# Kernel optimization log

Hardware: AMD Instinct MI355X
Metric: run time of the kernel (lower is better)

The kernel has to match this reference:

```python
import jax, jax.numpy as jnp
import numpy as np

N_USER = 100000
N_ITEM = 200000
N_NODES = N_USER + N_ITEM
NNZ = 4000000
EMB = 64
N_LAYERS = 3
BATCH = 4096


def setup_inputs() -> dict:
    key = jax.random.key(0)
    ks = jax.random.split(key, 12)
    inp = {
        'users': jax.random.randint(ks[0], (BATCH,), 0, N_USER, dtype=jnp.int32),
        'pos_items': jax.random.randint(ks[1], (BATCH,), 0, N_ITEM, dtype=jnp.int32),
        'neg_items': jax.random.randint(ks[2], (BATCH,), 0, N_ITEM, dtype=jnp.int32),
        'row': jax.random.randint(ks[3], (NNZ,), 0, N_NODES, dtype=jnp.int32),
        'col': jax.random.randint(ks[4], (NNZ,), 0, N_NODES, dtype=jnp.int32),
        'vals': jax.random.uniform(ks[5], (NNZ,), dtype=jnp.float32),
        'user_emb': 0.1 * jax.random.normal(ks[6], (N_USER, EMB), dtype=jnp.float32),
        'item_emb': 0.1 * jax.random.normal(ks[7], (N_ITEM, EMB), dtype=jnp.float32),
        'W_gc': 0.1 * jax.random.normal(ks[8], (N_LAYERS, EMB, EMB), dtype=jnp.float32),
        'b_gc': 0.1 * jax.random.normal(ks[9], (N_LAYERS, EMB), dtype=jnp.float32),
        'W_bi': 0.1 * jax.random.normal(ks[10], (N_LAYERS, EMB, EMB), dtype=jnp.float32),
        'b_bi': 0.1 * jax.random.normal(ks[11], (N_LAYERS, EMB), dtype=jnp.float32),
    }
    return inp


def _l2_normalize(x, eps=1e-12):
    # matches torch F.normalize(p=2, dim=1): x / max(||x||, eps)
    n = jnp.sqrt(jnp.sum(x * x, axis=1, keepdims=True))
    return x / jnp.maximum(n, eps)


def reference(users, pos_items, neg_items, row, col, vals, user_emb, item_emb, W_gc, b_gc, W_bi, b_bi):
    B = users.shape[0]
    # sparse adjacency propagation: side = A_hat @ [user_emb; item_emb]
    emb = jnp.concatenate([user_emb, item_emb], axis=0)          # [N, d]
    msgs = vals[:, None] * emb[col]                               # [nnz, d]
    side = jax.ops.segment_sum(msgs, row, num_segments=N_NODES)  # [N, d]

    u_side = side[users]                                          # [B, d]
    i_side = jnp.concatenate([side[N_USER + pos_items], side[N_USER + neg_items]], axis=0)
    small_side = jnp.concatenate([u_side, i_side], axis=0)        # [3B, d]
    ego = jnp.concatenate([user_emb[users], item_emb[pos_items], item_emb[neg_items]], axis=0)

    all_embeddings = [ego]
    for k in range(N_LAYERS):
        sum_e = small_side @ W_gc[k] + b_gc[k]
        bi = (ego * small_side) @ W_bi[k] + b_bi[k]
        ego = jax.nn.leaky_relu(sum_e + bi, negative_slope=0.2)
        all_embeddings.append(_l2_normalize(ego))

    all_e = jnp.concatenate(all_embeddings, axis=1)               # [3B, d*(L+1)]
    u_g = all_e[:B]
    i_g = all_e[B:]
    pos_g = i_g[:B]
    neg_g = i_g[B:]
    return (u_g, pos_g, neg_g)
```

## Files before the change

kernel.cpp:

```cpp
#include <hip/hip_runtime.h>

#define N_USER   100000
#define N_ITEM   200000
#define N_NODES  300000
#define NNZ      4000000
#define EMB      64
#define N_LAYERS 3
#define BATCH    4096
#define NSLOT    (3*BATCH)
#define MAXE     96
#define HCAP     768


__global__ void k_setup(const int* __restrict__ users,
                        const int* __restrict__ pos,
                        const int* __restrict__ neg,
                        int* __restrict__ slot_of_node,
                        int* __restrict__ count) {
    int i = blockIdx.x * blockDim.x + threadIdx.x;
    if (i >= NSLOT) return;
    count[i] = 0;
    int node;
    if (i < BATCH)            node = users[i];
    else if (i < 2 * BATCH)   node = N_USER + pos[i - BATCH];
    else                      node = N_USER + neg[i - 2 * BATCH];
    slot_of_node[node] = i;
}

__global__ void __launch_bounds__(256) k_build(
        const int* __restrict__ row,
        const int* __restrict__ col,
        const float* __restrict__ vals,
        const int* __restrict__ slot_of_node,
        int* __restrict__ count,
        int* __restrict__ csr_col,
        float* __restrict__ csr_val) {
    __shared__ int ls_e[HCAP];
    __shared__ int ls_s[HCAP];
    __shared__ int cnt;
    int tid = threadIdx.x;
    if (tid == 0) cnt = 0;
    __syncthreads();

    const int4* rows4 = (const int4*)row;
    const int nt4 = NNZ / 4;
    int base4 = blockIdx.x * 1024;

    int4 r[4]; bool ok[4];
    #pragma unroll
    for (int q = 0; q < 4; ++q) {
        int t = base4 + q * 256 + tid;
        ok[q] = t < nt4;
        r[q] = rows4[ok[q] ? t : 0];
    }
    int s[16];
    #pragma unroll
    for (int q = 0; q < 4; ++q) {
        s[q * 4 + 0] = slot_of_node[r[q].x];
        s[q * 4 + 1] = slot_of_node[r[q].y];
        s[q * 4 + 2] = slot_of_node[r[q].z];
        s[q * 4 + 3] = slot_of_node[r[q].w];
    }
    #pragma unroll
    for (int q = 0; q < 4; ++q) {
        if (!ok[q]) continue;
        int e = (base4 + q * 256 + tid) * 4;
        #pragma unroll
        for (int i = 0; i < 4; ++i) {
            int si = s[q * 4 + i];
            if (si >= 0) {
                int p = atomicAdd(&cnt, 1);
                if (p < HCAP) { ls_e[p] = e + i; ls_s[p] = si; }
                else {
                    int pp = atomicAdd(&count[si], 1);
                    if (pp < MAXE) {
                        csr_col[(size_t)si * MAXE + pp] = col[e + i];
                        csr_val[(size_t)si * MAXE + pp] = vals[e + i];
                    }
                }
            }
        }
    }
    __syncthreads();

    int n = cnt; n = (n < HCAP) ? n : HCAP;
    for (int t = tid; t < n; t += 256) {
        int e  = ls_e[t];
        int si = ls_s[t];
        int c  = col[e];
        float v = vals[e];
        int p = atomicAdd(&count[si], 1);
        if (p < MAXE) {
            csr_col[(size_t)si * MAXE + p] = c;
            csr_val[(size_t)si * MAXE + p] = v;
        }
    }
}

__global__ void __launch_bounds__(256) k_gather(
        const int* __restrict__ users,
        const int* __restrict__ pos,
        const int* __restrict__ neg,
        const float* __restrict__ user_emb,
        const float* __restrict__ item_emb,
        const int* __restrict__ slot_of_node,
        const int* __restrict__ count,
        const int* __restrict__ csr_col,
        const float* __restrict__ csr_val,
        float* __restrict__ side) {
    int tid = threadIdx.x;
    int w = tid >> 6;
    int j = tid & 63;
    int slot = blockIdx.x * 4 + w;

    int node;
    if (slot < BATCH)          node = users[slot];
    else if (slot < 2 * BATCH) node = N_USER + pos[slot - BATCH];
    else                       node = N_USER + neg[slot - 2 * BATCH];

    int wslot = slot_of_node[node];
    wslot = __builtin_amdgcn_readfirstlane(wslot);
    int n = count[wslot];
    n = (n < MAXE) ? n : MAXE;
    n = __builtin_amdgcn_readfirstlane(n);
    const int*   cc = csr_col + (size_t)wslot * MAXE;
    const float* cv = csr_val + (size_t)wslot * MAXE;

    float acc = 0.f;
    for (int t0 = 0; t0 < n; t0 += 16) {
        float vv[16];
        const float* ss[16];
        #pragma unroll
        for (int k = 0; k < 16; ++k) {
            int  t  = t0 + k;
            bool okk = t < n;
            int  idx = okk ? t : 0;
            int   c = cc[idx];
            float v = cv[idx];
            vv[k] = okk ? v : 0.f;
            ss[k] = (c < N_USER) ? (user_emb + (size_t)c * EMB)
                                 : (item_emb + (size_t)(c - N_USER) * EMB);
        }
        float gg[16];
        #pragma unroll
        for (int k = 0; k < 16; ++k) gg[k] = ss[k][j];
        #pragma unroll
        for (int k = 0; k < 16; ++k) acc = fmaf(vv[k], gg[k], acc);
    }
    side[(size_t)slot * EMB + j] = acc;
}

__global__ void __launch_bounds__(256) k_mlp(
        const int* __restrict__ users,
        const int* __restrict__ pos,
        const int* __restrict__ neg,
        const float* __restrict__ user_emb,
        const float* __restrict__ item_emb,
        const float* __restrict__ W_gc,
        const float* __restrict__ b_gc,
        const float* __restrict__ W_bi,
        const float* __restrict__ b_bi,
        const float* __restrict__ side,
        float* __restrict__ out) {
    __shared__ float wg[EMB * EMB];
    __shared__ float wb[EMB * EMB];
    int tid = threadIdx.x;
    int w = tid >> 6;
    int j = tid & 63;
    int sbase = blockIdx.x * 16 + w * 4;

    float sval[4], e[4];
    #pragma unroll
    for (int s = 0; s < 4; ++s) {
        int slot = sbase + s;
        int node;
        if (slot < BATCH)          node = users[slot];
        else if (slot < 2 * BATCH) node = N_USER + pos[slot - BATCH];
        else                       node = N_USER + neg[slot - 2 * BATCH];
        const float* erow = (node < N_USER) ? (user_emb + (size_t)node * EMB)
                                            : (item_emb + (size_t)(node - N_USER) * EMB);
        e[s]    = erow[j];
        sval[s] = side[(size_t)slot * EMB + j];
        out[(size_t)slot * 256 + j] = e[s];
    }

    for (int k = 0; k < N_LAYERS; ++k) {
        __syncthreads();
        {
            const float4* g4 = (const float4*)(W_gc + (size_t)k * EMB * EMB);
            const float4* b4 = (const float4*)(W_bi + (size_t)k * EMB * EMB);
            float4* lg = (float4*)wg;
            float4* lb = (float4*)wb;
            #pragma unroll
            for (int i2 = tid; i2 < EMB * EMB / 4; i2 += 256) { lg[i2] = g4[i2]; lb[i2] = b4[i2]; }
        }
        __syncthreads();

        float b1 = b_gc[k * EMB + j];
        float b2 = b_bi[k * EMB + j];
        float sum1[4], sum2[4], pv[4];
        #pragma unroll
        for (int s = 0; s < 4; ++s) { sum1[s] = b1; sum2[s] = b2; pv[s] = sval[s] * e[s]; }

        #pragma unroll 8
        for (int i = 0; i < EMB; ++i) {
            float wgi = wg[i * EMB + j];
            float wbi = wb[i * EMB + j];
            #pragma unroll
            for (int s = 0; s < 4; ++s) {
                float si = __uint_as_float(__builtin_amdgcn_readlane(__float_as_uint(sval[s]), i));
                float pi = __uint_as_float(__builtin_amdgcn_readlane(__float_as_uint(pv[s]),   i));
                sum1[s] = fmaf(si, wgi, sum1[s]);
                sum2[s] = fmaf(pi, wbi, sum2[s]);
            }
        }

        #pragma unroll
        for (int s = 0; s < 4; ++s) {
            float x = sum1[s] + sum2[s];
            x = (x >= 0.f) ? x : 0.2f * x;
            float sq = x * x;
            #pragma unroll
            for (int o = 32; o; o >>= 1) sq += __shfl_xor(sq, o, 64);
            float nn = fmaxf(sqrtf(sq), 1e-12f);
            out[(size_t)(sbase + s) * 256 + (k + 1) * 64 + j] = x / nn;
            e[s] = x;
        }
    }
}

extern "C" void kernel_launch(void* const* d_in, const int* in_sizes, int n_in,
                              void* d_out, int out_size, void* d_ws, size_t ws_size,
                              hipStream_t stream) {
    const int*   users    = (const int*)  d_in[0];
    const int*   pos      = (const int*)  d_in[1];
    const int*   neg      = (const int*)  d_in[2];
    const int*   row      = (const int*)  d_in[3];
    const int*   col      = (const int*)  d_in[4];
    const float* vals     = (const float*)d_in[5];
    const float* user_emb = (const float*)d_in[6];
    const float* item_emb = (const float*)d_in[7];
    const float* W_gc     = (const float*)d_in[8];
    const float* b_gc     = (const float*)d_in[9];
    const float* W_bi     = (const float*)d_in[10];
    const float* b_bi     = (const float*)d_in[11];
    float* out = (float*)d_out;

    char* ws = (char*)d_ws;
    int*   slot_of_node = (int*)ws;
    int*   count        = (int*)(ws + 1200128);
    int*   csr_col      = (int*)(ws + 1249280);
    float* csr_val      = (float*)(ws + 5967872);
    float* side         = (float*)(ws + 10686464);

    hipMemsetAsync(slot_of_node, 0xFF, (size_t)N_NODES * sizeof(int), stream);

    k_setup<<<(NSLOT + 255) / 256, 256, 0, stream>>>(users, pos, neg,
                                                     slot_of_node, count);
    k_build<<<(NNZ / 4 + 1023) / 1024, 256, 0, stream>>>(row, col, vals, slot_of_node,
                                                         count, csr_col, csr_val);
    k_gather<<<NSLOT / 4, 256, 0, stream>>>(users, pos, neg, user_emb, item_emb,
                                            slot_of_node, count, csr_col, csr_val,
                                            side);
    k_mlp<<<NSLOT / 16, 256, 0, stream>>>(users, pos, neg, user_emb, item_emb,
                                          W_gc, b_gc, W_bi, b_bi, side, out);
}
```

Measured before the change: 88.83 us.

## Shrink node-slot table to 16-bit, stream col/vals, interleave CSR, shuffle-broadcast gather

Result: faster. 81.87 us (-7.8%).

```diff
diff --git a/kernel.cpp b/kernel.cpp
--- a/kernel.cpp
+++ b/kernel.cpp
@@ -12,71 +12,83 @@
 #define HCAP     768
 
 
+#define TBL4   37500
+#define CNT4   3072
+
+__global__ void __launch_bounds__(256) k_clear(int4* __restrict__ table4,
+                                               int4* __restrict__ count4) {
+    int i = blockIdx.x * blockDim.x + threadIdx.x;
+    if (i < TBL4)              table4[i] = make_int4(-1, -1, -1, -1);
+    else if (i < TBL4 + CNT4)  count4[i - TBL4] = make_int4(0, 0, 0, 0);
+}
+
 __global__ void k_setup(const int* __restrict__ users,
                         const int* __restrict__ pos,
                         const int* __restrict__ neg,
-                        int* __restrict__ slot_of_node,
-                        int* __restrict__ count) {
+                        unsigned short* __restrict__ table16) {
     int i = blockIdx.x * blockDim.x + threadIdx.x;
     if (i >= NSLOT) return;
-    count[i] = 0;
     int node;
     if (i < BATCH)            node = users[i];
     else if (i < 2 * BATCH)   node = N_USER + pos[i - BATCH];
     else                      node = N_USER + neg[i - 2 * BATCH];
-    slot_of_node[node] = i;
+    table16[node] = (unsigned short)i;
 }
 
 __global__ void __launch_bounds__(256) k_build(
         const int* __restrict__ row,
         const int* __restrict__ col,
         const float* __restrict__ vals,
-        const int* __restrict__ slot_of_node,
+        const unsigned short* __restrict__ table16,
         int* __restrict__ count,
-        int* __restrict__ csr_col,
-        float* __restrict__ csr_val) {
-    __shared__ int ls_e[HCAP];
-    __shared__ int ls_s[HCAP];
-    __shared__ int cnt;
+        int2* __restrict__ csr2) {
+    __shared__ int   ls_s[HCAP];
+    __shared__ int   ls_c[HCAP];
+    __shared__ float ls_v[HCAP];
+    __shared__ int   cnt;
     int tid = threadIdx.x;
     if (tid == 0) cnt = 0;
     __syncthreads();
 
-    const int4* rows4 = (const int4*)row;
+    const int4*   rows4 = (const int4*)row;
+    const int4*   cols4 = (const int4*)col;
+    const float4* vals4 = (const float4*)vals;
     const int nt4 = NNZ / 4;
-    int base4 = blockIdx.x * 1024;
-
-    int4 r[4]; bool ok[4];
-    #pragma unroll
-    for (int q = 0; q < 4; ++q) {
+    int base4 = blockIdx.x * 512;
+
+    int4 r[2], c[2]; float4 v[2]; bool ok[2];
+    #pragma unroll
+    for (int q = 0; q < 2; ++q) {
         int t = base4 + q * 256 + tid;
         ok[q] = t < nt4;
-        r[q] = rows4[ok[q] ? t : 0];
-    }
-    int s[16];
-    #pragma unroll
-    for (int q = 0; q < 4; ++q) {
-        s[q * 4 + 0] = slot_of_node[r[q].x];
-        s[q * 4 + 1] = slot_of_node[r[q].y];
-        s[q * 4 + 2] = slot_of_node[r[q].z];
-        s[q * 4 + 3] = slot_of_node[r[q].w];
-    }
-    #pragma unroll
-    for (int q = 0; q < 4; ++q) {
+        int tt = ok[q] ? t : 0;
+        r[q] = rows4[tt];
+        c[q] = cols4[tt];
+        v[q] = vals4[tt];
+    }
+    int s[8];
+    #pragma unroll
+    for (int q = 0; q < 2; ++q) {
+        s[q * 4 + 0] = (int)(short)table16[r[q].x];
+        s[q * 4 + 1] = (int)(short)table16[r[q].y];
+        s[q * 4 + 2] = (int)(short)table16[r[q].z];
+        s[q * 4 + 3] = (int)(short)table16[r[q].w];
+    }
+    #pragma unroll
+    for (int q = 0; q < 2; ++q) {
         if (!ok[q]) continue;
-        int e = (base4 + q * 256 + tid) * 4;
+        int cc[4] = { c[q].x, c[q].y, c[q].z, c[q].w };
+        float vv[4] = { v[q].x, v[q].y, v[q].z, v[q].w };
         #pragma unroll
         for (int i = 0; i < 4; ++i) {
             int si = s[q * 4 + i];
             if (si >= 0) {
                 int p = atomicAdd(&cnt, 1);
-                if (p < HCAP) { ls_e[p] = e + i; ls_s[p] = si; }
+                if (p < HCAP) { ls_s[p] = si; ls_c[p] = cc[i]; ls_v[p] = vv[i]; }
                 else {
                     int pp = atomicAdd(&count[si], 1);
-                    if (pp < MAXE) {
-                        csr_col[(size_t)si * MAXE + pp] = col[e + i];
-                        csr_val[(size_t)si * MAXE + pp] = vals[e + i];
-                    }
+                    if (pp < MAXE)
+                        csr2[(size_t)si * MAXE + pp] = make_int2(cc[i], __float_as_int(vv[i]));
                 }
             }
         }
@@ -85,15 +97,10 @@
 
     int n = cnt; n = (n < HCAP) ? n : HCAP;
     for (int t = tid; t < n; t += 256) {
-        int e  = ls_e[t];
         int si = ls_s[t];
-        int c  = col[e];
-        float v = vals[e];
         int p = atomicAdd(&count[si], 1);
-        if (p < MAXE) {
-            csr_col[(size_t)si * MAXE + p] = c;
-            csr_val[(size_t)si * MAXE + p] = v;
-        }
+        if (p < MAXE)
+            csr2[(size_t)si * MAXE + p] = make_int2(ls_c[t], __float_as_int(ls_v[t]));
     }
 }
 
@@ -103,10 +110,9 @@
         const int* __restrict__ neg,
         const float* __restrict__ user_emb,
         const float* __restrict__ item_emb,
-        const int* __restrict__ slot_of_node,
+        const unsigned short* __restrict__ table16,
         const int* __restrict__ count,
-        const int* __restrict__ csr_col,
-        const float* __restrict__ csr_val,
+        const int2* __restrict__ csr2,
         float* __restrict__ side) {
     int tid = threadIdx.x;
     int w = tid >> 6;
@@ -118,34 +124,36 @@
     else if (slot < 2 * BATCH) node = N_USER + pos[slot - BATCH];
     else                       node = N_USER + neg[slot - 2 * BATCH];
 
-    int wslot = slot_of_node[node];
+    int wslot = (int)(short)table16[node];
     wslot = __builtin_amdgcn_readfirstlane(wslot);
     int n = count[wslot];
     n = (n < MAXE) ? n : MAXE;
     n = __builtin_amdgcn_readfirstlane(n);
-    const int*   cc = csr_col + (size_t)wslot * MAXE;
-    const float* cv = csr_val + (size_t)wslot * MAXE;
+    const int2* base = csr2 + (size_t)wslot * MAXE;
 
     float acc = 0.f;
-    for (int t0 = 0; t0 < n; t0 += 16) {
-        float vv[16];
-        const float* ss[16];
-        #pragma unroll
-        for (int k = 0; k < 16; ++k) {
-            int  t  = t0 + k;
-            bool okk = t < n;
-            int  idx = okk ? t : 0;
-            int   c = cc[idx];
-            float v = cv[idx];
-            vv[k] = okk ? v : 0.f;
-            ss[k] = (c < N_USER) ? (user_emb + (size_t)c * EMB)
-                                 : (item_emb + (size_t)(c - N_USER) * EMB);
-        }
-        float gg[16];
-        #pragma unroll
-        for (int k = 0; k < 16; ++k) gg[k] = ss[k][j];
-        #pragma unroll
-        for (int k = 0; k < 16; ++k) acc = fmaf(vv[k], gg[k], acc);
+    for (int t0 = 0; t0 < n; t0 += 64) {
+        int idx = t0 + j;
+        int2 ev = make_int2(0, 0);
+        if (idx < n) ev = base[idx];
+        int m = n - t0; m = (m < 64) ? m : 64;
+        for (int tt = 0; tt < m; tt += 16) {
+            float vv[16], gg[16];
+            #pragma unroll
+            for (int k = 0; k < 16; ++k) {
+                int  t  = tt + k;
+                bool okk = t < m;
+                int   cc = __shfl(ev.x, t, 64);
+                float vb = __uint_as_float((unsigned)__shfl(ev.y, t, 64));
+                vv[k] = okk ? vb : 0.f;
+                int ci = okk ? cc : 0;
+                const float* sp = (ci < N_USER) ? (user_emb + (size_t)ci * EMB)
+                                                : (item_emb + (size_t)(ci - N_USER) * EMB);
+                gg[k] = sp[j];
+            }
+            #pragma unroll
+            for (int k = 0; k < 16; ++k) acc = fmaf(vv[k], gg[k], acc);
+        }
     }
     side[(size_t)slot * EMB + j] = acc;
 }
@@ -247,21 +255,17 @@
     float* out = (float*)d_out;
 
     char* ws = (char*)d_ws;
-    int*   slot_of_node = (int*)ws;
-    int*   count        = (int*)(ws + 1200128);
-    int*   csr_col      = (int*)(ws + 1249280);
-    float* csr_val      = (float*)(ws + 5967872);
-    float* side         = (float*)(ws + 10686464);
-
-    hipMemsetAsync(slot_of_node, 0xFF, (size_t)N_NODES * sizeof(int), stream);
-
-    k_setup<<<(NSLOT + 255) / 256, 256, 0, stream>>>(users, pos, neg,
-                                                     slot_of_node, count);
-    k_build<<<(NNZ / 4 + 1023) / 1024, 256, 0, stream>>>(row, col, vals, slot_of_node,
-                                                         count, csr_col, csr_val);
+    unsigned short* table16 = (unsigned short*)ws;
+    int*            count   = (int*)(ws + 600064);
+    int2*           csr2    = (int2*)(ws + 649216);
+    float*          side    = (float*)(ws + 10086400);
+
+    k_clear<<<(TBL4 + CNT4 + 255) / 256, 256, 0, stream>>>((int4*)table16, (int4*)count);
+    k_setup<<<(NSLOT + 255) / 256, 256, 0, stream>>>(users, pos, neg, table16);
+    k_build<<<(NNZ / 4 + 511) / 512, 256, 0, stream>>>(row, col, vals, table16,
+                                                       count, csr2);
     k_gather<<<NSLOT / 4, 256, 0, stream>>>(users, pos, neg, user_emb, item_emb,
-                                            slot_of_node, count, csr_col, csr_val,
-                                            side);
+                                            table16, count, csr2, side);
     k_mlp<<<NSLOT / 16, 256, 0, stream>>>(users, pos, neg, user_emb, item_emb,
                                           W_gc, b_gc, W_bi, b_bi, side, out);
 }
```
